# Optimization experiments

Hardware: AMD Instinct MI355X
Metric: run time of the kernel (lower is better)

Reference implementation:

```python
import jax, jax.numpy as jnp
import numpy as np

N, E, IN, H, K = 50000, 800000, 64, 128, 16
EPS = 1e-15


def setup_inputs() -> dict:
    key = jax.random.key(0)
    ks = jax.random.split(key, 8)
    x = jax.random.normal(ks[0], (N, IN), jnp.float32)
    edge_index = jax.random.randint(ks[1], (2, E), 0, N)
    edge_weight = jax.random.uniform(ks[2], (E,), jnp.float32)
    # GCNConv(normalize=False) params: lin weight (no lin bias) + additive bias
    W1 = jax.random.normal(ks[3], (IN, H), jnp.float32) / np.sqrt(IN)
    b1 = jnp.zeros((H,), jnp.float32)
    W2 = jax.random.normal(ks[4], (H, H), jnp.float32) / np.sqrt(H)
    b2 = jnp.zeros((H,), jnp.float32)
    # MLP head: single Linear(H, K) since mlp_units=[]
    Wm = jax.random.normal(ks[5], (H, K), jnp.float32) / np.sqrt(H)
    bm = jnp.zeros((K,), jnp.float32)
    return {"x": x, "edge_index": edge_index, "edge_weight": edge_weight,
            "W1": W1, "b1": b1, "W2": W2, "b2": b2, "Wm": Wm, "bm": bm}


def _gcn(h_in, W, b, src, dst, w):
    # GCNConv with normalize=False, cached=False: no self-loops, no degree norm.
    # out_i = sum_{(j->i) in E} w_ji * (x_j @ W) + b
    h = h_in @ W                         # [N, out] dense transform first
    msg = h[src] * w[:, None]            # [E, out] gather + edge scale
    agg = jax.ops.segment_sum(msg, dst, num_segments=N)  # scatter-add
    return agg + b


def reference(x, edge_index, edge_weight, W1, b1, W2, b2, Wm, bm):
    src, dst = edge_index[0], edge_index[1]
    h = jax.nn.relu(_gcn(x, W1, b1, src, dst, edge_weight))
    h = jax.nn.relu(_gcn(h, W2, b2, src, dst, edge_weight))
    s = h @ Wm + bm                      # cluster logits [N, K]
    sm = jax.nn.softmax(s, axis=-1)      # soft assignments S
    # just_balance_pool balance loss: -trace(sqrt(S^T S + EPS)) elementwise-sqrt,
    # i.e. -sum_k sqrt(sum_i S_ik^2 + EPS), normalized by sqrt(N*K).
    diag = jnp.sum(sm * sm, axis=0)      # [K] = diag(S^T S)
    loss = -jnp.sum(jnp.sqrt(diag + EPS))
    loss = loss / jnp.sqrt(jnp.asarray(N * K, sm.dtype))
    return sm, loss
```

## Files before the change

kernel.cpp:

```cpp
#include <hip/hip_runtime.h>
#include <hip/hip_fp16.h>
#include <math.h>

static constexpr int N_NODES = 50000;
static constexpr int E_EDGES = 800000;
static constexpr int IN_F = 64;
static constexpr int H_F = 128;
static constexpr int K_C = 16;
static constexpr int BUCK_SHIFT = 7;
static constexpr int NBUCK = (N_NODES + 127) >> BUCK_SHIFT;
static constexpr int CHUNK_E = 4096;
static constexpr int NCHUNK = (E_EDGES + CHUNK_E - 1) / CHUNK_E;
static constexpr int BUCK_CAP = 4096;

typedef _Float16 h4 __attribute__((ext_vector_type(4)));
typedef _Float16 h8 __attribute__((ext_vector_type(8)));
typedef float f4 __attribute__((ext_vector_type(4)));

__device__ __forceinline__ void unpack(unsigned int e, int& s, float& w) {
  s = (int)(e & 0xffffu);
  w = __half2float(__ushort_as_half((unsigned short)(e >> 16)));
}

__global__ __launch_bounds__(256) void prep_kernel(
    const float* __restrict__ x, __half* __restrict__ xh,
    const float* __restrict__ W1, __half* __restrict__ WT1,
    const float* __restrict__ W2, __half* __restrict__ WT2,
    int* __restrict__ bcount, float* __restrict__ diag) {
  const int i = blockIdx.x * 256 + threadIdx.x;
  const int n4 = N_NODES * IN_F / 4;
  if (i < n4) {
    float4 v = ((const float4*)x)[i];
    __half2* o = (__half2*)xh + (size_t)i * 2;
    o[0] = __floats2half2_rn(v.x, v.y);
    o[1] = __floats2half2_rn(v.z, v.w);
  }
  const int j = i - n4;
  if (j >= 0 && j < IN_F * 128) {
    const int k = j >> 7, col = j & 127;
    unsigned boff = (unsigned)((col * IN_F + k) * 2) ^ (unsigned)((col & 7) << 4);
    *(__half*)((char*)WT1 + boff) = __float2half_rn(W1[j]);
  }
  const int k2 = j - IN_F * 128;
  if (k2 >= 0 && k2 < H_F * 128) {
    const int k = k2 >> 7, col = k2 & 127;
    unsigned boff = (unsigned)((col * H_F + k) * 2) ^ (unsigned)((col & 7) << 4);
    *(__half*)((char*)WT2 + boff) = __float2half_rn(W2[k2]);
  }
  if (i < NBUCK) bcount[i] = 0;
  if (i < K_C) diag[i] = 0.f;
}

__global__ __launch_bounds__(256) void bhist_kernel(
    const int* __restrict__ dst, int* __restrict__ bcount) {
  __shared__ int lh[NBUCK];
  for (int i = threadIdx.x; i < NBUCK; i += 256) lh[i] = 0;
  __syncthreads();
  const int e0 = blockIdx.x * CHUNK_E;
  const int cnt = min(CHUNK_E, E_EDGES - e0);
  for (int i = threadIdx.x; i < cnt; i += 256)
    atomicAdd(&lh[dst[e0 + i] >> BUCK_SHIFT], 1);
  __syncthreads();
  for (int i = threadIdx.x; i < NBUCK; i += 256)
    if (lh[i]) atomicAdd(&bcount[i], lh[i]);
}

__global__ __launch_bounds__(64) void bscan_kernel(
    const int* __restrict__ bcount, int* __restrict__ bbase, int* __restrict__ bcursor) {
  const int t = threadIdx.x;
  int carry = 0;
  for (int base = 0; base < NBUCK; base += 64) {
    const int idx = base + t;
    const int v = (idx < NBUCK) ? bcount[idx] : 0;
    int inc = v;
#pragma unroll
    for (int d = 1; d < 64; d <<= 1) {
      int u = __shfl_up(inc, d);
      if (t >= d) inc += u;
    }
    if (idx < NBUCK) {
      const int ex = carry + inc - v;
      bbase[idx] = ex;
      bcursor[idx] = ex;
    }
    carry += __shfl(inc, 63);
  }
  if (t == 0) bbase[NBUCK] = E_EDGES;
}

__global__ __launch_bounds__(256) void bin_pass(
    const int* __restrict__ src, const int* __restrict__ dst,
    const float* __restrict__ w, int* __restrict__ bcursor,
    int2* __restrict__ inter) {
  __shared__ int lhist[NBUCK];
  __shared__ int lstart[NBUCK];
  __shared__ int bbase_s[NBUCK];
  __shared__ int2 stage[CHUNK_E];
  const int e0 = blockIdx.x * CHUNK_E;
  const int cnt = min(CHUNK_E, E_EDGES - e0);

  for (int i = threadIdx.x; i < NBUCK; i += 256) lhist[i] = 0;
  __syncthreads();
  for (int i = threadIdx.x; i < cnt; i += 256)
    atomicAdd(&lhist[dst[e0 + i] >> BUCK_SHIFT], 1);
  __syncthreads();

  if (threadIdx.x < 64) {
    const int lane = threadIdx.x;
    int carry = 0;
    for (int base = 0; base < NBUCK; base += 64) {
      const int idx = base + lane;
      const int v = (idx < NBUCK) ? lhist[idx] : 0;
      int inc = v;
#pragma unroll
      for (int d = 1; d < 64; d <<= 1) {
        int u = __shfl_up(inc, d);
        if (lane >= d) inc += u;
      }
      if (idx < NBUCK) lstart[idx] = carry + inc - v;
      carry += __shfl(inc, 63);
    }
  }
  __syncthreads();

  for (int b = threadIdx.x; b < NBUCK; b += 256) {
    const int c = lhist[b];
    bbase_s[b] = (c > 0) ? atomicAdd(&bcursor[b], c) : 0;
    lhist[b] = lstart[b];
  }
  __syncthreads();

  for (int i = threadIdx.x; i < cnt; i += 256) {
    const int d = dst[e0 + i];
    const int b = d >> BUCK_SHIFT;
    const int pos = atomicAdd(&lhist[b], 1);
    const unsigned short wb = __half_as_ushort(__float2half_rn(w[e0 + i]));
    stage[pos] = make_int2(src[e0 + i] | ((d & 127) << 16),
                           (int)wb | (b << 16));
  }
  __syncthreads();

  for (int i = threadIdx.x; i < cnt; i += 256) {
    const int2 en = stage[i];
    const int b = (en.y >> 16) & 0x1ff;
    inter[bbase_s[b] + (i - lstart[b])] = en;
  }
}

__global__ __launch_bounds__(256) void sortoff_pass(
    const int2* __restrict__ inter, const int* __restrict__ bbase,
    unsigned int* __restrict__ csr, int* __restrict__ off) {
  __shared__ int lhist[128];
  __shared__ int lstart[128];
  __shared__ unsigned int outbuf[BUCK_CAP];
  const int b = blockIdx.x;
  const int n0 = b << BUCK_SHIFT;
  const int r0 = bbase[b];
  const int r1 = bbase[b + 1];
  const int cnt = r1 - r0;

  if (threadIdx.x < 128) lhist[threadIdx.x] = 0;
  __syncthreads();
  for (int i = threadIdx.x; i < cnt; i += 256)
    atomicAdd(&lhist[(inter[r0 + i].x >> 16) & 127], 1);
  __syncthreads();

  if (threadIdx.x < 64) {
    const int lane = threadIdx.x;
    int carry = 0;
#pragma unroll
    for (int base = 0; base < 128; base += 64) {
      const int v = lhist[base + lane];
      int inc = v;
#pragma unroll
      for (int d = 1; d < 64; d <<= 1) {
        int u = __shfl_up(inc, d);
        if (lane >= d) inc += u;
      }
      lstart[base + lane] = carry + inc - v;
      carry += __shfl(inc, 63);
    }
  }
  __syncthreads();

  if (threadIdx.x < 128) {
    const int nn = n0 + threadIdx.x;
    if (nn < N_NODES) off[nn] = r0 + lstart[threadIdx.x];
    lhist[threadIdx.x] = lstart[threadIdx.x];
  }
  if (b == NBUCK - 1 && threadIdx.x == 0) off[N_NODES] = E_EDGES;
  __syncthreads();

  for (int i = threadIdx.x; i < cnt; i += 256) {
    const int2 en = inter[r0 + i];
    const int dlo = (en.x >> 16) & 127;
    const int pos = atomicAdd(&lhist[dlo], 1);
    outbuf[pos] = (unsigned int)(en.x & 0xffff) |
                  ((unsigned int)(en.y & 0xffff) << 16);
  }
  __syncthreads();
  for (int i = threadIdx.x; i < cnt; i += 256) csr[r0 + i] = outbuf[i];
}

__global__ __launch_bounds__(256) void gather_x(
    const __half* __restrict__ t, const int* __restrict__ off,
    const unsigned int* __restrict__ csr, __half* __restrict__ outb) {
  const int node = blockIdx.x * 4 + (threadIdx.x >> 6);
  const int l = threadIdx.x & 63;
  const int g = l >> 4;
  const int f0 = (l & 15) * 4;
  const int p0 = off[node], p1 = off[node + 1];
  f4 a0 = {0.f, 0.f, 0.f, 0.f}, a1 = {0.f, 0.f, 0.f, 0.f};
  int p = p0;
  for (; p + 16 <= p1; p += 16) {
    int s[4]; float w[4]; h4 v[4];
#pragma unroll
    for (int u = 0; u < 4; ++u) unpack(csr[p + 4 * u + g], s[u], w[u]);
#pragma unroll
    for (int u = 0; u < 4; ++u) v[u] = *(const h4*)(t + (size_t)s[u] * IN_F + f0);
#pragma unroll
    for (int u = 0; u < 4; ++u) {
      f4& a = (u & 1) ? a1 : a0;
      a.x = fmaf((float)v[u].x, w[u], a.x); a.y = fmaf((float)v[u].y, w[u], a.y);
      a.z = fmaf((float)v[u].z, w[u], a.z); a.w = fmaf((float)v[u].w, w[u], a.w);
    }
  }
  for (; p + 8 <= p1; p += 8) {
    int s0, s1; float w0, w1;
    unpack(csr[p + g], s0, w0); unpack(csr[p + 4 + g], s1, w1);
    const h4 v0 = *(const h4*)(t + (size_t)s0 * IN_F + f0);
    const h4 v1 = *(const h4*)(t + (size_t)s1 * IN_F + f0);
    a0.x = fmaf((float)v0.x, w0, a0.x); a0.y = fmaf((float)v0.y, w0, a0.y);
    a0.z = fmaf((float)v0.z, w0, a0.z); a0.w = fmaf((float)v0.w, w0, a0.w);
    a1.x = fmaf((float)v1.x, w1, a1.x); a1.y = fmaf((float)v1.y, w1, a1.y);
    a1.z = fmaf((float)v1.z, w1, a1.z); a1.w = fmaf((float)v1.w, w1, a1.w);
  }
  for (; p < p1; p += 4) {
    const int idx = p + g;
    unsigned e = csr[min(idx, p1 - 1)];
    int s; float w;
    unpack(e, s, w);
    if (idx >= p1) w = 0.f;
    const h4 v = *(const h4*)(t + (size_t)s * IN_F + f0);
    a0.x = fmaf((float)v.x, w, a0.x); a0.y = fmaf((float)v.y, w, a0.y);
    a0.z = fmaf((float)v.z, w, a0.z); a0.w = fmaf((float)v.w, w, a0.w);
  }
  a0.x += a1.x; a0.y += a1.y; a0.z += a1.z; a0.w += a1.w;
  a0.x += __shfl_xor(a0.x, 16); a0.y += __shfl_xor(a0.y, 16);
  a0.z += __shfl_xor(a0.z, 16); a0.w += __shfl_xor(a0.w, 16);
  a0.x += __shfl_xor(a0.x, 32); a0.y += __shfl_xor(a0.y, 32);
  a0.z += __shfl_xor(a0.z, 32); a0.w += __shfl_xor(a0.w, 32);
  if (l < 16) {
    h4 o;
    o.x = (_Float16)a0.x; o.y = (_Float16)a0.y;
    o.z = (_Float16)a0.z; o.w = (_Float16)a0.w;
    *(h4*)(outb + (size_t)node * IN_F + f0) = o;
  }
}

template<int K, bool BIAS_RELU>
__global__ __launch_bounds__(256) void gemm_mfma(
    const __half* __restrict__ A, const __half* __restrict__ WT,
    const float* __restrict__ bias, __half* __restrict__ out, int n) {
  __shared__ _Float16 Wl[128 * K];
  for (int t = threadIdx.x; t < 128 * K / 8; t += 256)
    ((uint4*)Wl)[t] = ((const uint4*)WT)[t];
  __syncthreads();

  const int wv = threadIdx.x >> 6;
  const int l = threadIdx.x & 63;
  const int row = l & 15, kg = l >> 4;
  const int r0 = blockIdx.x * 64 + wv * 16;
  const int ar = min(r0 + row, n - 1);

  h8 af[K / 32];
#pragma unroll
  for (int ks = 0; ks < K / 32; ++ks)
    af[ks] = *(const h8*)(A + (size_t)ar * K + ks * 32 + kg * 8);

  const unsigned swz = (unsigned)((row & 7) << 4);
#pragma unroll
  for (int c = 0; c < 8; ++c) {
    const int col = c * 16 + row;
    f4 acc = {0.f, 0.f, 0.f, 0.f};
#pragma unroll
    for (int ks = 0; ks < K / 32; ++ks) {
      const unsigned boff = ((unsigned)((col * K + ks * 32 + kg * 8) * 2)) ^ swz;
      const h8 bf = *(const h8*)((const char*)Wl + boff);
      acc = __builtin_amdgcn_mfma_f32_16x16x32_f16(af[ks], bf, acc, 0, 0, 0);
    }
    const float bb = BIAS_RELU ? bias[col] : 0.f;
#pragma unroll
    for (int q = 0; q < 4; ++q) {
      const int rr = r0 + kg * 4 + q;
      if (rr < n) {
        float v = acc[q];
        if (BIAS_RELU) v = fmaxf(v + bb, 0.f);
        out[(size_t)rr * H_F + col] = __float2half_rn(v);
      }
    }
  }
}

__global__ __launch_bounds__(256) void gather_h(
    const __half* __restrict__ t, const int* __restrict__ off,
    const unsigned int* __restrict__ csr, __half* __restrict__ outb) {
  const int node = blockIdx.x * 4 + (threadIdx.x >> 6);
  const int lane = threadIdx.x & 63;
  const __half2* __restrict__ tb = (const __half2*)t;
  const int p0 = off[node], p1 = off[node + 1];
  float2 a[4];
#pragma unroll
  for (int i = 0; i < 4; ++i) a[i] = make_float2(0.f, 0.f);
  int p = p0;
  for (; p + 16 <= p1; p += 16) {
    int s[16]; float w[16]; __half2 hv[16];
#pragma unroll
    for (int i = 0; i < 16; ++i) unpack(csr[p + i], s[i], w[i]);
#pragma unroll
    for (int i = 0; i < 16; ++i) hv[i] = tb[(size_t)s[i] * 64 + lane];
#pragma unroll
    for (int i = 0; i < 16; ++i) {
      const float2 f = __half22float2(hv[i]);
      a[i & 3].x = fmaf(f.x, w[i], a[i & 3].x);
      a[i & 3].y = fmaf(f.y, w[i], a[i & 3].y);
    }
  }
  for (; p + 8 <= p1; p += 8) {
    int s[8]; float w[8]; __half2 hv[8];
#pragma unroll
    for (int i = 0; i < 8; ++i) unpack(csr[p + i], s[i], w[i]);
#pragma unroll
    for (int i = 0; i < 8; ++i) hv[i] = tb[(size_t)s[i] * 64 + lane];
#pragma unroll
    for (int i = 0; i < 8; ++i) {
      const float2 f = __half22float2(hv[i]);
      a[i & 3].x = fmaf(f.x, w[i], a[i & 3].x);
      a[i & 3].y = fmaf(f.y, w[i], a[i & 3].y);
    }
  }
  for (; p < p1; ++p) {
    int s; float w;
    unpack(csr[p], s, w);
    const float2 f = __half22float2(tb[(size_t)s * 64 + lane]);
    a[0].x = fmaf(f.x, w, a[0].x); a[0].y = fmaf(f.y, w, a[0].y);
  }
  const float2 s2 = make_float2((a[0].x + a[1].x) + (a[2].x + a[3].x),
                                (a[0].y + a[1].y) + (a[2].y + a[3].y));
  ((__half2*)outb)[(size_t)node * 64 + lane] = __float22half2_rn(s2);
}

__global__ __launch_bounds__(256) void head_kernel(
    const __half* __restrict__ h2raw, const float* __restrict__ b2,
    const float* __restrict__ Wm, const float* __restrict__ bm,
    float* __restrict__ sm_out, float* __restrict__ diag, int n) {
  __shared__ float Wl[H_F * K_C];
  __shared__ float b2l[H_F];
  __shared__ float part[K_C];
  for (int t = threadIdx.x; t < H_F * K_C; t += 256) Wl[t] = Wm[t];
  if (threadIdx.x < H_F) b2l[threadIdx.x] = b2[threadIdx.x];
  if (threadIdx.x < K_C) part[threadIdx.x] = 0.f;
  __syncthreads();

  const int node = blockIdx.x * 256 + threadIdx.x;
  const int lane = threadIdx.x & 63;
  float acc[K_C];
#pragma unroll
  for (int c = 0; c < K_C; ++c) acc[c] = bm[c];

  if (node < n) {
    const __half2* __restrict__ hrow = (const __half2*)(h2raw + (size_t)node * H_F);
#pragma unroll 4
    for (int k2 = 0; k2 < H_F / 2; ++k2) {
      const float2 hv = __half22float2(hrow[k2]);
      const float h0 = fmaxf(hv.x + b2l[2 * k2], 0.f);
      const float h1 = fmaxf(hv.y + b2l[2 * k2 + 1], 0.f);
      const float4* __restrict__ w0 = (const float4*)(Wl + (2 * k2) * K_C);
      const float4* __restrict__ w1 = (const float4*)(Wl + (2 * k2 + 1) * K_C);
#pragma unroll
      for (int q = 0; q < 4; ++q) {
        const float4 aa = w0[q], bb = w1[q];
        acc[4 * q + 0] = fmaf(h0, aa.x, acc[4 * q + 0]);
        acc[4 * q + 1] = fmaf(h0, aa.y, acc[4 * q + 1]);
        acc[4 * q + 2] = fmaf(h0, aa.z, acc[4 * q + 2]);
        acc[4 * q + 3] = fmaf(h0, aa.w, acc[4 * q + 3]);
        acc[4 * q + 0] = fmaf(h1, bb.x, acc[4 * q + 0]);
        acc[4 * q + 1] = fmaf(h1, bb.y, acc[4 * q + 1]);
        acc[4 * q + 2] = fmaf(h1, bb.z, acc[4 * q + 2]);
        acc[4 * q + 3] = fmaf(h1, bb.w, acc[4 * q + 3]);
      }
    }
  }

  float mx = acc[0];
#pragma unroll
  for (int c = 1; c < K_C; ++c) mx = fmaxf(mx, acc[c]);
  float sum = 0.f;
#pragma unroll
  for (int c = 0; c < K_C; ++c) { acc[c] = __expf(acc[c] - mx); sum += acc[c]; }
  const float inv = 1.f / sum;
  float sq[K_C];
  if (node < n) {
#pragma unroll
    for (int c = 0; c < K_C; ++c) { acc[c] *= inv; sq[c] = acc[c] * acc[c]; }
    float4* o = (float4*)(sm_out + (size_t)node * K_C);
    o[0] = make_float4(acc[0], acc[1], acc[2], acc[3]);
    o[1] = make_float4(acc[4], acc[5], acc[6], acc[7]);
    o[2] = make_float4(acc[8], acc[9], acc[10], acc[11]);
    o[3] = make_float4(acc[12], acc[13], acc[14], acc[15]);
  } else {
#pragma unroll
    for (int c = 0; c < K_C; ++c) sq[c] = 0.f;
  }

#pragma unroll
  for (int c = 0; c < K_C; ++c) {
    float v = sq[c];
#pragma unroll
    for (int off2 = 32; off2; off2 >>= 1) v += __shfl_xor(v, off2);
    if (lane == 0) atomicAdd(&part[c], v);
  }
  __syncthreads();
  if (threadIdx.x < K_C) atomicAdd(&diag[threadIdx.x], part[threadIdx.x]);
}

__global__ void loss_kernel(const float* __restrict__ diag, float* __restrict__ out) {
  int c = threadIdx.x;
  float v = (c < K_C) ? sqrtf(diag[c] + 1e-15f) : 0.f;
#pragma unroll
  for (int off2 = 8; off2; off2 >>= 1) v += __shfl_xor(v, off2, 16);
  if (c == 0) out[0] = -v / sqrtf((float)N_NODES * (float)K_C);
}

extern "C" void kernel_launch(void* const* d_in, const int* in_sizes, int n_in,
                              void* d_out, int out_size, void* d_ws, size_t ws_size,
                              hipStream_t stream) {
  const float* x  = (const float*)d_in[0];
  const int*   ei = (const int*)d_in[1];
  const float* ew = (const float*)d_in[2];
  const float* W1 = (const float*)d_in[3];
  const float* b1 = (const float*)d_in[4];
  const float* W2 = (const float*)d_in[5];
  const float* b2 = (const float*)d_in[6];
  const float* Wm = (const float*)d_in[7];
  const float* bm = (const float*)d_in[8];
  float* out = (float*)d_out;

  const int* srcv = ei;
  const int* dstv = ei + E_EDGES;

  char* ws = (char*)d_ws;
  float*        diag    = (float*)ws;
  int*          bcount  = (int*)(ws + 256);
  int*          bbase   = (int*)(ws + 2048);
  int*          bcursor = (int*)(ws + 4096);
  __half*       WT1     = (__half*)(ws + 8192);
  __half*       WT2     = (__half*)(ws + 8192 + 16384);
  int*          off     = (int*)(ws + 65536);
  unsigned int* csr     = (unsigned int*)(off + N_NODES + 64);
  int2*         inter   = (int2*)(csr + E_EDGES);
  char*         bufA    = (char*)(inter + E_EDGES);
  char*         bufB    = bufA + (size_t)N_NODES * H_F * 2;

  __half* xh    = (__half*)bufB;
  __half* aggxh = (__half*)bufA;
  __half* h1h   = (__half*)bufB;
  __half* t2h   = (__half*)bufA;
  __half* h2h   = (__half*)bufB;

  prep_kernel<<<3221, 256, 0, stream>>>(x, xh, W1, WT1, W2, WT2, bcount, diag);

  bhist_kernel<<<NCHUNK, 256, 0, stream>>>(dstv, bcount);
  bscan_kernel<<<1, 64, 0, stream>>>(bcount, bbase, bcursor);
  bin_pass<<<NCHUNK, 256, 0, stream>>>(srcv, dstv, ew, bcursor, inter);
  sortoff_pass<<<NBUCK, 256, 0, stream>>>(inter, bbase, csr, off);

  gather_x<<<N_NODES / 4, 256, 0, stream>>>(xh, off, csr, aggxh);
  gemm_mfma<IN_F, true><<<(N_NODES + 63) / 64, 256, 0, stream>>>(aggxh, WT1, b1, h1h, N_NODES);

  gemm_mfma<H_F, false><<<(N_NODES + 63) / 64, 256, 0, stream>>>(h1h, WT2, nullptr, t2h, N_NODES);
  gather_h<<<N_NODES / 4, 256, 0, stream>>>(t2h, off, csr, h2h);

  head_kernel<<<(N_NODES + 255) / 256, 256, 0, stream>>>(h2h, b2, Wm, bm, out, diag, N_NODES);
  loss_kernel<<<1, 64, 0, stream>>>(diag, out + (size_t)N_NODES * K_C);
}
```

Measured before the change: 153.5 us.

## Split layer-2 gather into two feature planes to shrink gathered working set

The second GEMM now writes its output in planar form, as two contiguous 64-feature halves of N×64 each. The layer-2 gather becomes two launches, one per half. In each launch a wavefront splits into two 32-lane groups that handle alternating edges, and the groups are combined with a shuffle. The intent is to make each gather's random-access working set half the size (6.4MB) so it fits better in cache and gets a higher L2/LLC hit rate. The cost is reading the CSR twice, an extra launch, and narrower 128-byte row fetches.

```diff
diff --git a/kernel.cpp b/kernel.cpp
--- a/kernel.cpp
+++ b/kernel.cpp
@@ -258,7 +258,7 @@
   }
 }
 
-template<int K, bool BIAS_RELU>
+template<int K, bool BIAS_RELU, bool PLANAR>
 __global__ __launch_bounds__(256) void gemm_mfma(
     const __half* __restrict__ A, const __half* __restrict__ WT,
     const float* __restrict__ bias, __half* __restrict__ out, int n) {
@@ -296,42 +296,37 @@
       if (rr < n) {
         float v = acc[q];
         if (BIAS_RELU) v = fmaxf(v + bb, 0.f);
-        out[(size_t)rr * H_F + col] = __float2half_rn(v);
+        if (PLANAR) {
+          out[(size_t)(col >> 6) * ((size_t)N_NODES * 64) +
+              (size_t)rr * 64 + (col & 63)] = __float2half_rn(v);
+        } else {
+          out[(size_t)rr * H_F + col] = __float2half_rn(v);
+        }
       }
     }
   }
 }
 
-__global__ __launch_bounds__(256) void gather_h(
-    const __half* __restrict__ t, const int* __restrict__ off,
-    const unsigned int* __restrict__ csr, __half* __restrict__ outb) {
+__global__ __launch_bounds__(256) void gather_h2(
+    const __half* __restrict__ plane,
+    const int* __restrict__ off, const unsigned int* __restrict__ csr,
+    __half* __restrict__ outb) {
   const int node = blockIdx.x * 4 + (threadIdx.x >> 6);
-  const int lane = threadIdx.x & 63;
-  const __half2* __restrict__ tb = (const __half2*)t;
+  const int l = threadIdx.x & 63;
+  const int g = l >> 5;
+  const int cl = l & 31;
+  const __half2* __restrict__ tb = (const __half2*)plane;
   const int p0 = off[node], p1 = off[node + 1];
   float2 a[4];
 #pragma unroll
   for (int i = 0; i < 4; ++i) a[i] = make_float2(0.f, 0.f);
   int p = p0;
   for (; p + 16 <= p1; p += 16) {
-    int s[16]; float w[16]; __half2 hv[16];
-#pragma unroll
-    for (int i = 0; i < 16; ++i) unpack(csr[p + i], s[i], w[i]);
-#pragma unroll
-    for (int i = 0; i < 16; ++i) hv[i] = tb[(size_t)s[i] * 64 + lane];
-#pragma unroll
-    for (int i = 0; i < 16; ++i) {
-      const float2 f = __half22float2(hv[i]);
-      a[i & 3].x = fmaf(f.x, w[i], a[i & 3].x);
-      a[i & 3].y = fmaf(f.y, w[i], a[i & 3].y);
-    }
-  }
-  for (; p + 8 <= p1; p += 8) {
     int s[8]; float w[8]; __half2 hv[8];
 #pragma unroll
-    for (int i = 0; i < 8; ++i) unpack(csr[p + i], s[i], w[i]);
-#pragma unroll
-    for (int i = 0; i < 8; ++i) hv[i] = tb[(size_t)s[i] * 64 + lane];
+    for (int i = 0; i < 8; ++i) unpack(csr[p + 2 * i + g], s[i], w[i]);
+#pragma unroll
+    for (int i = 0; i < 8; ++i) hv[i] = tb[(size_t)s[i] * 32 + cl];
 #pragma unroll
     for (int i = 0; i < 8; ++i) {
       const float2 f = __half22float2(hv[i]);
@@ -339,15 +334,34 @@
       a[i & 3].y = fmaf(f.y, w[i], a[i & 3].y);
     }
   }
-  for (; p < p1; ++p) {
+  for (; p + 8 <= p1; p += 8) {
+    int s[4]; float w[4]; __half2 hv[4];
+#pragma unroll
+    for (int i = 0; i < 4; ++i) unpack(csr[p + 2 * i + g], s[i], w[i]);
+#pragma unroll
+    for (int i = 0; i < 4; ++i) hv[i] = tb[(size_t)s[i] * 32 + cl];
+#pragma unroll
+    for (int i = 0; i < 4; ++i) {
+      const float2 f = __half22float2(hv[i]);
+      a[i & 3].x = fmaf(f.x, w[i], a[i & 3].x);
+      a[i & 3].y = fmaf(f.y, w[i], a[i & 3].y);
+    }
+  }
+  for (; p < p1; p += 2) {
+    const int idx = p + g;
+    unsigned e = csr[min(idx, p1 - 1)];
     int s; float w;
-    unpack(csr[p], s, w);
-    const float2 f = __half22float2(tb[(size_t)s * 64 + lane]);
+    unpack(e, s, w);
+    if (idx >= p1) w = 0.f;
+    const float2 f = __half22float2(tb[(size_t)s * 32 + cl]);
     a[0].x = fmaf(f.x, w, a[0].x); a[0].y = fmaf(f.y, w, a[0].y);
   }
-  const float2 s2 = make_float2((a[0].x + a[1].x) + (a[2].x + a[3].x),
-                                (a[0].y + a[1].y) + (a[2].y + a[3].y));
-  ((__half2*)outb)[(size_t)node * 64 + lane] = __float22half2_rn(s2);
+  float2 s2 = make_float2((a[0].x + a[1].x) + (a[2].x + a[3].x),
+                          (a[0].y + a[1].y) + (a[2].y + a[3].y));
+  s2.x += __shfl_xor(s2.x, 32);
+  s2.y += __shfl_xor(s2.y, 32);
+  if (l < 32)
+    ((__half2*)(outb + (size_t)node * H_F))[cl] = __float22half2_rn(s2);
 }
 
 __global__ __launch_bounds__(256) void head_kernel(
@@ -465,7 +479,7 @@
   __half* xh    = (__half*)bufB;
   __half* aggxh = (__half*)bufA;
   __half* h1h   = (__half*)bufB;
-  __half* t2h   = (__half*)bufA;
+  __half* t2p   = (__half*)bufA;
   __half* h2h   = (__half*)bufB;
 
   prep_kernel<<<3221, 256, 0, stream>>>(x, xh, W1, WT1, W2, WT2, bcount, diag);
@@ -476,10 +490,11 @@
   sortoff_pass<<<NBUCK, 256, 0, stream>>>(inter, bbase, csr, off);
 
   gather_x<<<N_NODES / 4, 256, 0, stream>>>(xh, off, csr, aggxh);
-  gemm_mfma<IN_F, true><<<(N_NODES + 63) / 64, 256, 0, stream>>>(aggxh, WT1, b1, h1h, N_NODES);
-
-  gemm_mfma<H_F, false><<<(N_NODES + 63) / 64, 256, 0, stream>>>(h1h, WT2, nullptr, t2h, N_NODES);
-  gather_h<<<N_NODES / 4, 256, 0, stream>>>(t2h, off, csr, h2h);
+  gemm_mfma<IN_F, true, false><<<(N_NODES + 63) / 64, 256, 0, stream>>>(aggxh, WT1, b1, h1h, N_NODES);
+
+  gemm_mfma<H_F, false, true><<<(N_NODES + 63) / 64, 256, 0, stream>>>(h1h, WT2, nullptr, t2p, N_NODES);
+  gather_h2<<<N_NODES / 4, 256, 0, stream>>>(t2p, off, csr, h2h);
+  gather_h2<<<N_NODES / 4, 256, 0, stream>>>(t2p + (size_t)N_NODES * 64, off, csr, h2h + 64);
 
   head_kernel<<<(N_NODES + 255) / 256, 256, 0, stream>>>(h2h, b2, Wm, bm, out, diag, N_NODES);
   loss_kernel<<<1, 64, 0, stream>>>(diag, out + (size_t)N_NODES * K_C);
```

Measured after the change: 162.3 us. 1.06x slower.
